# Kernel optimization log

Measured on AMD Instinct MI355X. Metric: run time of the kernel, lower is better.

The kernel has to match this reference:

```python
import jax, jax.numpy as jnp
import numpy as np

N_NODES = 100000
N_EDGES = 600000
D_IN = 128
D_HID = 128
D_OUT = 128


def gcn_conv(x, W, b, src, dst, deg_inv_sqrt, num_nodes):
    # PyG GCNConv: h = x @ W, then symmetric-normalized scatter-add over edges
    # (edge list already includes self-loops; deg_inv_sqrt precomputed).
    h = x @ W  # [N, d_out]
    norm = deg_inv_sqrt[src] * deg_inv_sqrt[dst]  # [E+N]
    msgs = h[src] * norm[:, None]  # gather + scale, [E+N, d_out]
    out = jax.ops.segment_sum(msgs, dst, num_segments=num_nodes)
    return out + b


def setup_inputs() -> dict:
    key = jax.random.key(0)
    ks = jax.random.split(key, 8)
    x = jax.random.normal(ks[0], (N_NODES, D_IN), dtype=jnp.float32)
    edge_index = jax.random.randint(ks[1], (2, N_EDGES), 0, N_NODES, dtype=jnp.int32)
    def glorot(k, fan_in, fan_out):
        s = jnp.sqrt(6.0 / (fan_in + fan_out))
        return jax.random.uniform(k, (fan_in, fan_out), jnp.float32, -s, s)
    return {
        "x": x,
        "edge_index": edge_index,
        "W1": glorot(ks[2], D_IN, D_HID), "b1": jnp.zeros((D_HID,), jnp.float32),
        "W2": glorot(ks[3], D_HID, D_HID), "b2": jnp.zeros((D_HID,), jnp.float32),
        "W3": glorot(ks[4], D_HID, D_OUT), "b3": jnp.zeros((D_OUT,), jnp.float32),
    }


def reference(x, edge_index, W1, b1, W2, b2, W3, b3):
    n = x.shape[0]
    loops = jnp.arange(n, dtype=edge_index.dtype)
    src = jnp.concatenate([edge_index[0], loops])  # [E+N]
    dst = jnp.concatenate([edge_index[1], loops])
    # degree over destination nodes (edge weight 1), as in PyG gcn_norm
    deg = jax.ops.segment_sum(jnp.ones_like(dst, dtype=x.dtype), dst, num_segments=n)
    deg_inv_sqrt = jnp.where(deg > 0, jax.lax.rsqrt(jnp.maximum(deg, 1.0)), 0.0)

    h = gcn_conv(x, W1, b1, src, dst, deg_inv_sqrt, n)
    h = jax.nn.relu(h)  # dropout = identity in eval mode
    h = gcn_conv(h, W2, b2, src, dst, deg_inv_sqrt, n)
    h = jax.nn.relu(h)
    out = gcn_conv(h, W3, b3, src, dst, deg_inv_sqrt, n)
    return out
```

## Files before the change

kernel.cpp:

```cpp
#include <hip/hip_runtime.h>

#define D 128
#define SB 256
#define SI 8
#define SCHUNK (SB * SI)

typedef __attribute__((ext_vector_type(8))) short bf16x8;
typedef __attribute__((ext_vector_type(4))) float f32x4;
typedef unsigned int uint32;
typedef unsigned short ushort;

__device__ __forceinline__ ushort bf16rne(float f) {
  uint32 u = __float_as_uint(f);
  uint32 r = u + 0x7FFFu + ((u >> 16) & 1u);
  return (ushort)(r >> 16);
}
__device__ __forceinline__ float bf2f_lo(uint32 h) { return __uint_as_float(h << 16); }
__device__ __forceinline__ float bf2f_hi(uint32 h) { return __uint_as_float(h & 0xFFFF0000u); }
__device__ __forceinline__ uint32 packbf2(float x, float y) {
  return (uint32)bf16rne(x) | ((uint32)bf16rne(y) << 16);
}
__device__ __forceinline__ void acc8(float* a, float w, uint4 h) {
  a[0] += w * bf2f_lo(h.x); a[1] += w * bf2f_hi(h.x);
  a[2] += w * bf2f_lo(h.y); a[3] += w * bf2f_hi(h.y);
  a[4] += w * bf2f_lo(h.z); a[5] += w * bf2f_hi(h.z);
  a[6] += w * bf2f_lo(h.w); a[7] += w * bf2f_hi(h.w);
}


__global__ void count_kernel(const int* __restrict__ dst, int* __restrict__ cnt, int E) {
  int e = blockIdx.x * blockDim.x + threadIdx.x;
  if (e < E) atomicAdd(&cnt[dst[e]], 1);
}

__global__ void scan1_kernel(const int* __restrict__ cnt, int* __restrict__ off,
                             int* __restrict__ bsum, float* __restrict__ dis, int n) {
  __shared__ int tsum[SB];
  int tid = threadIdx.x;
  int base = blockIdx.x * SCHUNK;
  int v[SI];
  int s = 0;
#pragma unroll
  for (int i = 0; i < SI; i++) {
    int idx = base + tid * SI + i;
    v[i] = (idx < n) ? cnt[idx] : 0;
    s += v[i];
  }
  tsum[tid] = s;
  __syncthreads();
  for (int o = 1; o < SB; o <<= 1) {
    int t = (tid >= o) ? tsum[tid - o] : 0;
    __syncthreads();
    tsum[tid] += t;
    __syncthreads();
  }
  int run = tsum[tid] - s;
#pragma unroll
  for (int i = 0; i < SI; i++) {
    int idx = base + tid * SI + i;
    if (idx < n) {
      off[idx] = run;
      dis[idx] = rsqrtf((float)(v[i] + 1));
    }
    run += v[i];
  }
  if (tid == SB - 1) bsum[blockIdx.x] = tsum[tid];
}

__global__ void scan2_kernel(int* bsum, int nb) {
  if (threadIdx.x == 0 && blockIdx.x == 0) {
    int run = 0;
    for (int b = 0; b < nb; b++) { int t = bsum[b]; bsum[b] = run; run += t; }
  }
}

__global__ void scan3_kernel(int* __restrict__ off, const int* __restrict__ bsum,
                             int n, int total) {
  int i = blockIdx.x * blockDim.x + threadIdx.x;
  if (i < n) off[i] += bsum[i / SCHUNK];
  if (i == 0) off[n] = total;
}

__global__ void fill_kernel(const int* __restrict__ src, const int* __restrict__ dst,
                            const int* __restrict__ off, int* __restrict__ cnt,
                            uint2* __restrict__ epack, const float* __restrict__ dis, int E) {
  int e = blockIdx.x * blockDim.x + threadIdx.x;
  if (e >= E) return;
  int s = src[e], d = dst[e];
  int slot = atomicSub(&cnt[d], 1) - 1;
  int p = off[d] + slot;
  uint2 v;
  v.x = (uint32)s;
  v.y = __float_as_uint(dis[s] * dis[d]);
  epack[p] = v;
}


__global__ void wconv3_kernel(const float* __restrict__ W1, const float* __restrict__ W2,
                              const float* __restrict__ W3, ushort* __restrict__ Wf) {
  int idx = blockIdx.x * 256 + threadIdx.x;
  int which = idx >> 15;
  int id = idx & 32767;
  const float* W = (which == 0) ? W1 : ((which == 1) ? W2 : W3);
  int j = id & 7;
  int l = (id >> 3) & 63;
  int f = id >> 9;
  int p = f & 1, kc = (f >> 1) & 3, ct = f >> 3;
  int k = kc * 32 + (l >> 4) * 8 + j;
  int col = ct * 16 + (l & 15);
  float w = W[k * D + col];
  ushort hi = bf16rne(w);
  ushort outv = hi;
  if (p) {
    float hf = __uint_as_float((uint32)hi << 16);
    outv = bf16rne(w - hf);
  }
  Wf[idx] = outv;
}


__global__ void xb_kernel(const float* __restrict__ x, ushort* __restrict__ xb, int total4) {
  int i = blockIdx.x * 256 + threadIdx.x;
  if (i >= total4) return;
  float4 v = ((const float4*)x)[i];
  uint2 o;
  o.x = packbf2(v.x, v.y);
  o.y = packbf2(v.z, v.w);
  ((uint2*)xb)[i] = o;
}


template <int FINAL>
__global__ __launch_bounds__(256) void fused_kernel(const ushort* __restrict__ t,
                                                    const uint2* __restrict__ epack,
                                                    const int* __restrict__ off,
                                                    const float* __restrict__ dis,
                                                    const ushort* __restrict__ Wf,
                                                    const float* __restrict__ bias,
                                                    void* __restrict__ outp, int N) {
  __shared__ char lds[32768];
  int tid = threadIdx.x;
  int row0 = blockIdx.x * 64;
  int lane = tid & 63, wv = tid >> 6;
  int q = lane & 15, g = lane >> 4;
  const char* tb = (const char*)t;

#pragma unroll 1
  for (int n4 = 0; n4 < 4; n4++) {
    int r = wv * 16 + n4 * 4 + g;
    int node = row0 + r;
    float a[8];
#pragma unroll
    for (int i = 0; i < 8; i++) a[i] = 0.f;

    if (node < N) {
      int j0 = off[node], j1 = off[node + 1];
      int j = j0;
      for (; j + 4 <= j1; j += 4) {
        uint2 e0 = epack[j], e1 = epack[j + 1], e2 = epack[j + 2], e3 = epack[j + 3];
        uint4 h0 = *(const uint4*)(tb + (size_t)e0.x * 256 + q * 16);
        uint4 h1 = *(const uint4*)(tb + (size_t)e1.x * 256 + q * 16);
        uint4 h2 = *(const uint4*)(tb + (size_t)e2.x * 256 + q * 16);
        uint4 h3 = *(const uint4*)(tb + (size_t)e3.x * 256 + q * 16);
        acc8(a, __uint_as_float(e0.y), h0);
        acc8(a, __uint_as_float(e1.y), h1);
        acc8(a, __uint_as_float(e2.y), h2);
        acc8(a, __uint_as_float(e3.y), h3);
      }
      for (; j < j1; j++) {
        uint2 e0 = epack[j];
        uint4 h0 = *(const uint4*)(tb + (size_t)e0.x * 256 + q * 16);
        acc8(a, __uint_as_float(e0.y), h0);
      }
      float dsv = dis[node];
      float sw = dsv * dsv;
      uint4 hs = *(const uint4*)(tb + (size_t)node * 256 + q * 16);
      acc8(a, sw, hs);
    }
    uint4 pv;
    pv.x = packbf2(a[0], a[1]);
    pv.y = packbf2(a[2], a[3]);
    pv.z = packbf2(a[4], a[5]);
    pv.w = packbf2(a[6], a[7]);
    int boff = (r * 256 + q * 16) ^ ((r & 7) << 4);
    *(uint4*)(lds + boff) = pv;
  }
  __syncthreads();

  int lr = lane & 15, lg = lane >> 4;
  int m0 = wv * 16;

  bf16x8 af[4];
#pragma unroll
  for (int kc = 0; kc < 4; kc++) {
    int row = m0 + lr;
    int boff = (row * 256 + kc * 64 + lg * 16) ^ ((row & 7) << 4);
    af[kc] = *(bf16x8*)(lds + boff);
  }

  float bcol[8];
#pragma unroll
  for (int ct = 0; ct < 8; ct++) bcol[ct] = bias[ct * 16 + lr];

  f32x4 acc[8];
#pragma unroll
  for (int ct = 0; ct < 8; ct++) acc[ct] = (f32x4){0.f, 0.f, 0.f, 0.f};

#pragma unroll 1
  for (int ct = 0; ct < 8; ct++) {
    bf16x8 bf_[4][2];
#pragma unroll
    for (int kc = 0; kc < 4; kc++)
#pragma unroll
      for (int p = 0; p < 2; p++)
        bf_[kc][p] = *(const bf16x8*)&Wf[(size_t)((((ct * 4 + kc) * 2 + p) * 64 + lane) * 8)];
#pragma unroll
    for (int kc = 0; kc < 4; kc++) {
      acc[ct] = __builtin_amdgcn_mfma_f32_16x16x32_bf16(af[kc], bf_[kc][0], acc[ct], 0, 0, 0);
      acc[ct] = __builtin_amdgcn_mfma_f32_16x16x32_bf16(af[kc], bf_[kc][1], acc[ct], 0, 0, 0);
    }
  }
  __syncthreads();

  if (FINAL) {
#pragma unroll
    for (int ct = 0; ct < 8; ct++)
#pragma unroll
      for (int r = 0; r < 4; r++) {
        int row = m0 + lg * 4 + r;
        int col = ct * 16 + lr;
        float v = acc[ct][r] + bcol[ct];
        int boff = (row * 512 + col * 4) ^ ((row & 7) << 4);
        *(float*)(lds + boff) = v;
      }
    __syncthreads();
    float* out = (float*)outp;
#pragma unroll
    for (int i = 0; i < 8; i++) {
      int f = i * 4096 + tid * 16;
      int row = f >> 9;
      int boff = f ^ ((row & 7) << 4);
      if (row0 + row < N) {
        uint4 v = *(uint4*)(lds + boff);
        *(uint4*)((char*)out + (size_t)(row0 + row) * 512 + (f & 511)) = v;
      }
    }
  } else {
#pragma unroll
    for (int ct = 0; ct < 8; ct++)
#pragma unroll
      for (int r = 0; r < 4; r++) {
        int row = m0 + lg * 4 + r;
        int col = ct * 16 + lr;
        float v = fmaxf(acc[ct][r] + bcol[ct], 0.f);
        int boff = (row * 256 + col * 2) ^ ((row & 7) << 4);
        *(ushort*)(lds + boff) = bf16rne(v);
      }
    __syncthreads();
    ushort* outb = (ushort*)outp;
#pragma unroll
    for (int i = 0; i < 4; i++) {
      int f = i * 4096 + tid * 16;
      int row = f >> 8;
      int boff = f ^ ((row & 7) << 4);
      if (row0 + row < N) {
        uint4 v = *(uint4*)(lds + boff);
        *(uint4*)((char*)outb + (size_t)(row0 + row) * 256 + (f & 255)) = v;
      }
    }
  }
}


extern "C" void kernel_launch(void* const* d_in, const int* in_sizes, int n_in,
                              void* d_out, int out_size, void* d_ws, size_t ws_size,
                              hipStream_t stream) {
  const float* x  = (const float*)d_in[0];
  const int*   ei = (const int*)d_in[1];
  const float* W1 = (const float*)d_in[2];
  const float* b1 = (const float*)d_in[3];
  const float* W2 = (const float*)d_in[4];
  const float* b2 = (const float*)d_in[5];
  const float* W3 = (const float*)d_in[6];
  const float* b3 = (const float*)d_in[7];
  int N = in_sizes[0] / D;
  int E = in_sizes[1] / 2;
  const int* srcp = ei;
  const int* dstp = ei + E;

  char* wp = (char*)d_ws;
  auto carve = [&](size_t bytes) {
    void* p = (void*)wp;
    wp += (bytes + 255) & ~(size_t)255;
    return p;
  };
  int*    cnt   = (int*)carve((size_t)N * 4);
  int*    off   = (int*)carve((size_t)(N + 1) * 4);
  int*    bsum  = (int*)carve(256 * 4);
  float*  dis   = (float*)carve((size_t)N * 4);
  uint2*  epack = (uint2*)carve((size_t)E * 8);
  ushort* xb    = (ushort*)carve((size_t)N * D * 2);
  ushort* t1    = (ushort*)carve((size_t)N * D * 2);
  ushort* t2    = (ushort*)carve((size_t)N * D * 2);
  ushort* wfall = (ushort*)carve((size_t)3 * 32768 * 2);
  ushort* wf1 = wfall, *wf2 = wfall + 32768, *wf3 = wfall + 65536;

  hipMemsetAsync(cnt, 0, (size_t)N * 4, stream);

  const int tb = 256;
  wconv3_kernel<<<384, 256, 0, stream>>>(W1, W2, W3, wfall);
  xb_kernel<<<(N * D / 4 + 255) / 256, 256, 0, stream>>>(x, xb, N * D / 4);
  count_kernel<<<(E + tb - 1) / tb, tb, 0, stream>>>(dstp, cnt, E);
  int nb = (N + SCHUNK - 1) / SCHUNK;
  scan1_kernel<<<nb, SB, 0, stream>>>(cnt, off, bsum, dis, N);
  scan2_kernel<<<1, 64, 0, stream>>>(bsum, nb);
  scan3_kernel<<<(N + tb - 1) / tb, tb, 0, stream>>>(off, bsum, N, E);
  fill_kernel<<<(E + tb - 1) / tb, tb, 0, stream>>>(srcp, dstp, off, cnt, epack, dis, E);

  int fb = (N + 63) / 64;
  fused_kernel<0><<<fb, 256, 0, stream>>>(xb, epack, off, dis, wf1, b1, t1, N);
  fused_kernel<0><<<fb, 256, 0, stream>>>(t1, epack, off, dis, wf2, b2, t2, N);
  fused_kernel<1><<<fb, 256, 0, stream>>>(t2, epack, off, dis, wf3, b3, d_out, N);
}
```

Before: 263.3 us.

## Merge prep kernels, halve LDS, pipeline edge loads in gather loop

Merges the weight conversion, x-to-bf16 conversion and degree count kernels into one launch, cutting launch overhead. The fused GCN kernel drops its LDS from 32KB to 16KB by writing the final fp32 output in two halves, and adds launch_bounds occupancy hints. The edge gather loop prefetches the next four edge records while the current ones are being accumulated, padding the tail with zero-weight self entries and using 32-bit offsets. The risk is extra barriers in the final store, extra padded loads for low-degree nodes, and possible register pressure from the occupancy bound.

```diff
diff --git a/kernel.cpp b/kernel.cpp
--- a/kernel.cpp
+++ b/kernel.cpp
@@ -28,10 +28,47 @@
 }
 
 
-__global__ void count_kernel(const int* __restrict__ dst, int* __restrict__ cnt, int E) {
-  int e = blockIdx.x * blockDim.x + threadIdx.x;
-  if (e < E) atomicAdd(&cnt[dst[e]], 1);
-}
+__global__ void prep_kernel(const float* __restrict__ x, ushort* __restrict__ xb, int total4,
+                            const int* __restrict__ dst, int* __restrict__ cnt, int E,
+                            const float* __restrict__ W1, const float* __restrict__ W2,
+                            const float* __restrict__ W3, ushort* __restrict__ Wf,
+                            int xbB, int cntB) {
+  int b = blockIdx.x;
+  int tid = threadIdx.x;
+  if (b < xbB) {
+    int i = b * 256 + tid;
+    if (i < total4) {
+      float4 v = ((const float4*)x)[i];
+      uint2 o;
+      o.x = packbf2(v.x, v.y);
+      o.y = packbf2(v.z, v.w);
+      ((uint2*)xb)[i] = o;
+    }
+  } else if (b < xbB + cntB) {
+    int e = (b - xbB) * 256 + tid;
+    if (e < E) atomicAdd(&cnt[dst[e]], 1);
+  } else {
+    int idx = (b - xbB - cntB) * 256 + tid;
+    int which = idx >> 15;
+    int id = idx & 32767;
+    const float* W = (which == 0) ? W1 : ((which == 1) ? W2 : W3);
+    int j = id & 7;
+    int l = (id >> 3) & 63;
+    int f = id >> 9;
+    int p = f & 1, kc = (f >> 1) & 3, ct = f >> 3;
+    int k = kc * 32 + (l >> 4) * 8 + j;
+    int col = ct * 16 + (l & 15);
+    float w = W[k * D + col];
+    ushort hi = bf16rne(w);
+    ushort outv = hi;
+    if (p) {
+      float hf = __uint_as_float((uint32)hi << 16);
+      outv = bf16rne(w - hf);
+    }
+    Wf[idx] = outv;
+  }
+}
+
 
 __global__ void scan1_kernel(const int* __restrict__ cnt, int* __restrict__ off,
                              int* __restrict__ bsum, float* __restrict__ dis, int n) {
@@ -96,53 +133,20 @@
 }
 
 
-__global__ void wconv3_kernel(const float* __restrict__ W1, const float* __restrict__ W2,
-                              const float* __restrict__ W3, ushort* __restrict__ Wf) {
-  int idx = blockIdx.x * 256 + threadIdx.x;
-  int which = idx >> 15;
-  int id = idx & 32767;
-  const float* W = (which == 0) ? W1 : ((which == 1) ? W2 : W3);
-  int j = id & 7;
-  int l = (id >> 3) & 63;
-  int f = id >> 9;
-  int p = f & 1, kc = (f >> 1) & 3, ct = f >> 3;
-  int k = kc * 32 + (l >> 4) * 8 + j;
-  int col = ct * 16 + (l & 15);
-  float w = W[k * D + col];
-  ushort hi = bf16rne(w);
-  ushort outv = hi;
-  if (p) {
-    float hf = __uint_as_float((uint32)hi << 16);
-    outv = bf16rne(w - hf);
-  }
-  Wf[idx] = outv;
-}
-
-
-__global__ void xb_kernel(const float* __restrict__ x, ushort* __restrict__ xb, int total4) {
-  int i = blockIdx.x * 256 + threadIdx.x;
-  if (i >= total4) return;
-  float4 v = ((const float4*)x)[i];
-  uint2 o;
-  o.x = packbf2(v.x, v.y);
-  o.y = packbf2(v.z, v.w);
-  ((uint2*)xb)[i] = o;
-}
-
-
 template <int FINAL>
-__global__ __launch_bounds__(256) void fused_kernel(const ushort* __restrict__ t,
-                                                    const uint2* __restrict__ epack,
-                                                    const int* __restrict__ off,
-                                                    const float* __restrict__ dis,
-                                                    const ushort* __restrict__ Wf,
-                                                    const float* __restrict__ bias,
-                                                    void* __restrict__ outp, int N) {
-  __shared__ char lds[32768];
+__global__ __launch_bounds__(256, 4) void fused_kernel(const ushort* __restrict__ t,
+                                                       const uint2* __restrict__ epack,
+                                                       const int* __restrict__ off,
+                                                       const float* __restrict__ dis,
+                                                       const ushort* __restrict__ Wf,
+                                                       const float* __restrict__ bias,
+                                                       void* __restrict__ outp, int N) {
+  __shared__ char lds[16384];
   int tid = threadIdx.x;
   int row0 = blockIdx.x * 64;
   int lane = tid & 63, wv = tid >> 6;
   int q = lane & 15, g = lane >> 4;
+  int qb = q * 16;
   const char* tb = (const char*)t;
 
 #pragma unroll 1
@@ -154,27 +158,33 @@
     for (int i = 0; i < 8; i++) a[i] = 0.f;
 
     if (node < N) {
+      uint32 soff = ((uint32)node << 8) + qb;
+      uint4 hs = *(const uint4*)(tb + soff);
       int j0 = off[node], j1 = off[node + 1];
-      int j = j0;
-      for (; j + 4 <= j1; j += 4) {
-        uint2 e0 = epack[j], e1 = epack[j + 1], e2 = epack[j + 2], e3 = epack[j + 3];
-        uint4 h0 = *(const uint4*)(tb + (size_t)e0.x * 256 + q * 16);
-        uint4 h1 = *(const uint4*)(tb + (size_t)e1.x * 256 + q * 16);
-        uint4 h2 = *(const uint4*)(tb + (size_t)e2.x * 256 + q * 16);
-        uint4 h3 = *(const uint4*)(tb + (size_t)e3.x * 256 + q * 16);
-        acc8(a, __uint_as_float(e0.y), h0);
-        acc8(a, __uint_as_float(e1.y), h1);
-        acc8(a, __uint_as_float(e2.y), h2);
-        acc8(a, __uint_as_float(e3.y), h3);
-      }
-      for (; j < j1; j++) {
-        uint2 e0 = epack[j];
-        uint4 h0 = *(const uint4*)(tb + (size_t)e0.x * 256 + q * 16);
-        acc8(a, __uint_as_float(e0.y), h0);
-      }
       float dsv = dis[node];
       float sw = dsv * dsv;
-      uint4 hs = *(const uint4*)(tb + (size_t)node * 256 + q * 16);
+
+      auto ldE = [&](int idx) -> uint2 {
+        if (idx < j1) return epack[idx];
+        uint2 z; z.x = (uint32)node; z.y = 0u; return z;
+      };
+      int j = j0;
+      uint2 e0 = ldE(j), e1 = ldE(j + 1), e2 = ldE(j + 2), e3 = ldE(j + 3);
+      while (j < j1) {
+        uint4 h0 = *(const uint4*)(tb + ((e0.x << 8) + qb));
+        uint4 h1 = *(const uint4*)(tb + ((e1.x << 8) + qb));
+        uint4 h2 = *(const uint4*)(tb + ((e2.x << 8) + qb));
+        uint4 h3 = *(const uint4*)(tb + ((e3.x << 8) + qb));
+        float w0 = __uint_as_float(e0.y), w1 = __uint_as_float(e1.y);
+        float w2 = __uint_as_float(e2.y), w3 = __uint_as_float(e3.y);
+        int jn = j + 4;
+        e0 = ldE(jn); e1 = ldE(jn + 1); e2 = ldE(jn + 2); e3 = ldE(jn + 3);
+        acc8(a, w0, h0);
+        acc8(a, w1, h1);
+        acc8(a, w2, h2);
+        acc8(a, w3, h3);
+        j = jn;
+      }
       acc8(a, sw, hs);
     }
     uint4 pv;
@@ -182,7 +192,7 @@
     pv.y = packbf2(a[2], a[3]);
     pv.z = packbf2(a[4], a[5]);
     pv.w = packbf2(a[6], a[7]);
-    int boff = (r * 256 + q * 16) ^ ((r & 7) << 4);
+    int boff = (r * 256 + qb) ^ ((r & 7) << 4);
     *(uint4*)(lds + boff) = pv;
   }
   __syncthreads();
@@ -223,27 +233,33 @@
   __syncthreads();
 
   if (FINAL) {
-#pragma unroll
-    for (int ct = 0; ct < 8; ct++)
-#pragma unroll
-      for (int r = 0; r < 4; r++) {
-        int row = m0 + lg * 4 + r;
-        int col = ct * 16 + lr;
-        float v = acc[ct][r] + bcol[ct];
-        int boff = (row * 512 + col * 4) ^ ((row & 7) << 4);
-        *(float*)(lds + boff) = v;
-      }
-    __syncthreads();
     float* out = (float*)outp;
 #pragma unroll
-    for (int i = 0; i < 8; i++) {
-      int f = i * 4096 + tid * 16;
-      int row = f >> 9;
-      int boff = f ^ ((row & 7) << 4);
-      if (row0 + row < N) {
-        uint4 v = *(uint4*)(lds + boff);
-        *(uint4*)((char*)out + (size_t)(row0 + row) * 512 + (f & 511)) = v;
-      }
+    for (int p = 0; p < 2; p++) {
+#pragma unroll
+      for (int c4 = 0; c4 < 4; c4++) {
+        int ct = p * 4 + c4;
+#pragma unroll
+        for (int r = 0; r < 4; r++) {
+          int row = m0 + lg * 4 + r;
+          int colb = c4 * 16 + lr;
+          float v = acc[ct][r] + bcol[ct];
+          int boff = (row * 256 + colb * 4) ^ ((row & 7) << 4);
+          *(float*)(lds + boff) = v;
+        }
+      }
+      __syncthreads();
+#pragma unroll
+      for (int i = 0; i < 4; i++) {
+        int f = i * 4096 + tid * 16;
+        int row = f >> 8;
+        int boff = f ^ ((row & 7) << 4);
+        if (row0 + row < N) {
+          uint4 v = *(uint4*)(lds + boff);
+          *(uint4*)((char*)out + (size_t)(row0 + row) * 512 + p * 256 + (f & 255)) = v;
+        }
+      }
+      if (p == 0) __syncthreads();
     }
   } else {
 #pragma unroll
@@ -308,9 +324,11 @@
   hipMemsetAsync(cnt, 0, (size_t)N * 4, stream);
 
   const int tb = 256;
-  wconv3_kernel<<<384, 256, 0, stream>>>(W1, W2, W3, wfall);
-  xb_kernel<<<(N * D / 4 + 255) / 256, 256, 0, stream>>>(x, xb, N * D / 4);
-  count_kernel<<<(E + tb - 1) / tb, tb, 0, stream>>>(dstp, cnt, E);
+  int total4 = N * D / 4;
+  int xbB = (total4 + 255) / 256;
+  int cntB = (E + 255) / 256;
+  prep_kernel<<<xbB + cntB + 384, 256, 0, stream>>>(x, xb, total4, dstp, cnt, E,
+                                                    W1, W2, W3, wfall, xbB, cntB);
   int nb = (N + SCHUNK - 1) / SCHUNK;
   scan1_kernel<<<nb, SB, 0, stream>>>(cnt, off, bsum, dis, N);
   scan2_kernel<<<1, 64, 0, stream>>>(bsum, nb);
```

Measured after the change: 232.7 us. 11.6% less time.
